# Kernel tuning notes

Measured on AMD Instinct MI355X. Metric: run time of the kernel, lower is better.

The kernel has to match this reference:

```python
import jax, jax.numpy as jnp
import numpy as np

N_NODES = 8192
N_PAIRS = 524288
MAX_PATH = 5
D_FEAT = 128


def setup_inputs() -> dict:
    key = jax.random.key(0)
    k_x, k_b, k_src, k_dst, k_len = jax.random.split(key, 5)
    x = jax.random.normal(k_x, (N_NODES, D_FEAT), dtype=jnp.float32)
    b = jax.random.normal(k_b, (MAX_PATH,), dtype=jnp.float32)
    src = jax.random.randint(k_src, (N_PAIRS,), 0, N_NODES, dtype=jnp.int32)
    dst = jax.random.randint(k_dst, (N_PAIRS,), 0, N_NODES, dtype=jnp.int32)
    path_len = jax.random.randint(k_len, (N_PAIRS,), 0, 10, dtype=jnp.int32)
    return {"x": x, "b": b, "src": src, "dst": dst, "path_len": path_len}


def reference(x, b, src, dst, path_len):
    # bucket index = min(len(path), max_path_distance) - 1, clipped into [0, MAX_PATH-1]
    bucket = jnp.clip(jnp.minimum(path_len, MAX_PATH) - 1, 0, MAX_PATH - 1)
    vals = b[bucket]  # [n_pairs] gather from tiny bias table
    num_nodes = x.shape[0]
    spatial_matrix = jnp.zeros((num_nodes, num_nodes), dtype=jnp.float32)
    # single batched scatter replaces the per-edge python loop
    spatial_matrix = spatial_matrix.at[src, dst].set(vals)
    return spatial_matrix
```

## Files before the change

kernel.cpp:

```cpp
#include <hip/hip_runtime.h>


#define N_NODES   8192
#define N_PAIRS   524288
#define MAX_PATH  5
#define NTHR      256
#define TAG       0xC0000000u

typedef unsigned int u32;

__device__ __forceinline__ int bucket_of(int pl) {
    int b = min(pl, MAX_PATH) - 1;
    return max(0, min(b, MAX_PATH - 1));
}

__device__ __forceinline__ u32 pack_of(u32 pri, int bkt) {
    return TAG | (pri << 3) | (u32)bkt;
}

__global__ __launch_bounds__(NTHR) void scatter_pass(
        const int* __restrict__ src,
        const int* __restrict__ dst,
        const int* __restrict__ plen,
        u32* __restrict__ out_u) {
    const int t = blockIdx.x * NTHR + threadIdx.x;
    const int s = src[t];
    const int d = dst[t];
    const int p = plen[t];
    atomicMax(&out_u[s * N_NODES + d], pack_of((u32)t + 1u, bucket_of(p)));
}

__global__ __launch_bounds__(NTHR) void resolve_pass(
        const int* __restrict__ src,
        const int* __restrict__ dst,
        const float* __restrict__ b,
        u32* __restrict__ out_u,
        float* __restrict__ out_f) {
    const int t = blockIdx.x * NTHR + threadIdx.x;
    const int c = src[t] * N_NODES + dst[t];
    const u32 w = out_u[c];
    if ((w & ~7u) == (TAG | (((u32)t + 1u) << 3)))
        __builtin_nontemporal_store(b[w & 7u], &out_f[c]);
}

extern "C" void kernel_launch(void* const* d_in, const int* in_sizes, int n_in,
                              void* d_out, int out_size, void* d_ws, size_t ws_size,
                              hipStream_t stream) {
    const float* b   = (const float*)d_in[1];
    const int* src   = (const int*)d_in[2];
    const int* dst   = (const int*)d_in[3];
    const int* plen  = (const int*)d_in[4];

    float* out_f = (float*)d_out;
    u32*   out_u = (u32*)d_out;

    const int blocks = N_PAIRS / NTHR;
    scatter_pass<<<blocks, NTHR, 0, stream>>>(src, dst, plen, out_u);
    resolve_pass<<<blocks, NTHR, 0, stream>>>(src, dst, b, out_u, out_f);
}
```

Before: 331.0 us.

## Bin pairs by source row and resolve duplicates in shared memory

Replaces the global atomicMax-into-output plus read-back with a two-stage scheme. First, each pair is appended into a fixed-capacity per-source-row bucket in workspace, using atomic counters. Second, one block per row deduplicates destinations with shared-memory atomicMax and stores only the winning bias. This avoids random global atomics and read-modify-write traffic on the large output matrix. The costs are counter contention, a memset, a workspace round trip, and a fixed per-row capacity of 256 that silently drops pairs if exceeded.

```diff
diff --git a/kernel.cpp b/kernel.cpp
--- a/kernel.cpp
+++ b/kernel.cpp
@@ -5,56 +5,71 @@
 #define N_PAIRS   524288
 #define MAX_PATH  5
 #define NTHR      256
-#define TAG       0xC0000000u
+#define CAP       256
+#define CNT_BYTES (N_NODES * 4)
 
 typedef unsigned int u32;
+typedef unsigned long long u64;
 
 __device__ __forceinline__ int bucket_of(int pl) {
     int b = min(pl, MAX_PATH) - 1;
     return max(0, min(b, MAX_PATH - 1));
 }
 
-__device__ __forceinline__ u32 pack_of(u32 pri, int bkt) {
-    return TAG | (pri << 3) | (u32)bkt;
-}
-
-__global__ __launch_bounds__(NTHR) void scatter_pass(
+__global__ __launch_bounds__(NTHR) void bin_pass(
         const int* __restrict__ src,
         const int* __restrict__ dst,
         const int* __restrict__ plen,
-        u32* __restrict__ out_u) {
+        u32* __restrict__ cnt,
+        u64* __restrict__ entries) {
     const int t = blockIdx.x * NTHR + threadIdx.x;
     const int s = src[t];
-    const int d = dst[t];
-    const int p = plen[t];
-    atomicMax(&out_u[s * N_NODES + d], pack_of((u32)t + 1u, bucket_of(p)));
+    const u32 pack = (((u32)t + 1u) << 3) | (u32)bucket_of(plen[t]);
+    const u32 slot = atomicAdd(&cnt[s], 1u);
+    if (slot < CAP)
+        entries[((u32)s << 8) + slot] = ((u64)pack << 13) | (u32)dst[t];
 }
 
-__global__ __launch_bounds__(NTHR) void resolve_pass(
-        const int* __restrict__ src,
-        const int* __restrict__ dst,
+__global__ __launch_bounds__(NTHR) void row_pass(
+        const u32* __restrict__ cnt,
+        const u64* __restrict__ entries,
         const float* __restrict__ b,
-        u32* __restrict__ out_u,
         float* __restrict__ out_f) {
-    const int t = blockIdx.x * NTHR + threadIdx.x;
-    const int c = src[t] * N_NODES + dst[t];
-    const u32 w = out_u[c];
-    if ((w & ~7u) == (TAG | (((u32)t + 1u) << 3)))
-        __builtin_nontemporal_store(b[w & 7u], &out_f[c]);
+    __shared__ u32 img[N_NODES];
+    const int row = blockIdx.x;
+    const u32 n = min(cnt[row], (u32)CAP);
+    if (n == 0u) return;
+
+    const u32 i = threadIdx.x;
+    int d = 0;
+    u32 pack = 0;
+    if (i < n) {
+        const u64 e = entries[((u32)row << 8) + i];
+        d    = (int)(e & (u64)(N_NODES - 1));
+        pack = (u32)(e >> 13);
+        img[d] = 0u;
+    }
+    __syncthreads();
+    if (i < n) atomicMax(&img[d], pack);
+    __syncthreads();
+    if (i < n && img[d] == pack)
+        __builtin_nontemporal_store(b[pack & 7u], &out_f[row * N_NODES + d]);
 }
 
 extern "C" void kernel_launch(void* const* d_in, const int* in_sizes, int n_in,
                               void* d_out, int out_size, void* d_ws, size_t ws_size,
                               hipStream_t stream) {
-    const float* b   = (const float*)d_in[1];
-    const int* src   = (const int*)d_in[2];
-    const int* dst   = (const int*)d_in[3];
-    const int* plen  = (const int*)d_in[4];
+    const float* b  = (const float*)d_in[1];
+    const int* src  = (const int*)d_in[2];
+    const int* dst  = (const int*)d_in[3];
+    const int* plen = (const int*)d_in[4];
 
+    u32* cnt     = (u32*)d_ws;
+    u64* entries = (u64*)((char*)d_ws + CNT_BYTES);
     float* out_f = (float*)d_out;
-    u32*   out_u = (u32*)d_out;
 
-    const int blocks = N_PAIRS / NTHR;
-    scatter_pass<<<blocks, NTHR, 0, stream>>>(src, dst, plen, out_u);
-    resolve_pass<<<blocks, NTHR, 0, stream>>>(src, dst, b, out_u, out_f);
+    hipMemsetAsync(d_ws, 0, CNT_BYTES, stream);
+
+    bin_pass<<<N_PAIRS / NTHR, NTHR, 0, stream>>>(src, dst, plen, cnt, entries);
+    row_pass<<<N_NODES, NTHR, 0, stream>>>(cnt, entries, b, out_f);
 }
```

New measurement: 282.9 us. 1.17x faster.
